# Optimization experiments

Measured on AMD Instinct MI355X. Metric: run time of the kernel, lower is better.

Reference implementation:

```python
import jax, jax.numpy as jnp
import numpy as np

E = 128      # embedding_dim
H = 128      # hidden_dim
A = 4        # n_ary
DEPTH = 8    # complete 4-ary tree depth (root at level 0)
N_NODES = (A ** (DEPTH + 1) - 1) // (A - 1)  # 87381


def setup_inputs() -> dict:
    key = jax.random.key(0)
    ks = jax.random.split(key, 11)
    s = 0.05  # weight scale to keep gates in a sane range
    return {
        "embeddings": jax.random.normal(ks[0], (N_NODES, E), jnp.float32),
        "W_iou": jax.random.normal(ks[1], (3 * H, E), jnp.float32) * s,
        "b_iou": jax.random.normal(ks[2], (3 * H,), jnp.float32) * s,
        "U_iou": jax.random.normal(ks[3], (3 * H, A * H), jnp.float32) * s,
        "b_uiou": jax.random.normal(ks[4], (3 * H,), jnp.float32) * s,
        "W_f": jax.random.normal(ks[5], (H, E), jnp.float32) * s,
        "b_wf": jax.random.normal(ks[6], (H,), jnp.float32) * s,
        "U_f": jax.random.normal(ks[7], (A * H, A * H), jnp.float32) * s,
        "b_uf": jax.random.normal(ks[8], (A * H,), jnp.float32) * s,
        "h0": jax.random.uniform(ks[9], (1, A * H), jnp.float32),
        "c0": jax.random.uniform(ks[10], (1, A * H), jnp.float32),
    }


def _tree_lstm_cell(x, h, c, W_iou, b_iou, U_iou, b_uiou, W_f, b_wf, U_f, b_uf):
    # x: [n, E], h/c: [n, A*H]
    n = x.shape[0]
    iou = x @ W_iou.T + b_iou + h @ U_iou.T + b_uiou          # [n, 3H]
    i, o, u = jnp.split(iou, 3, axis=1)
    # forget gates: one per child slot, broadcast W_f(x) over arity dim
    f = jax.nn.sigmoid((h @ U_f.T + b_uf).reshape(n, A, H)
                       + (x @ W_f.T + b_wf)[:, None, :])       # [n, A, H]
    c_new = jax.nn.sigmoid(i) * jnp.tanh(u) + jnp.sum(f * c.reshape(n, A, H), axis=1)
    h_new = jax.nn.sigmoid(o) * jnp.tanh(c_new)
    return h_new, c_new


def reference(embeddings, W_iou, b_iou, U_iou, b_uiou, W_f, b_wf, U_f, b_uf, h0, c0):
    # Level-synchronized bottom-up pass over a complete 4-ary tree of depth DEPTH.
    # embeddings are ordered deepest-level-first; children of parent i at level l
    # are nodes 4i..4i+3 of level l+1.
    hs, cs = [], []
    off = 0
    n_leaf = A ** DEPTH
    h_in = jnp.tile(h0, (n_leaf, 1))  # leaves use learned initial state
    c_in = jnp.tile(c0, (n_leaf, 1))
    for l in range(DEPTH, -1, -1):
        n = A ** l
        x = embeddings[off:off + n]
        h_new, c_new = _tree_lstm_cell(x, h_in, c_in,
                                       W_iou, b_iou, U_iou, b_uiou,
                                       W_f, b_wf, U_f, b_uf)
        hs.append(h_new)
        cs.append(c_new)
        off += n
        if l > 0:
            # pack each parent's A children states into one [A*H] vector
            h_in = h_new.reshape(n // A, A * H)
            c_in = c_new.reshape(n // A, A * H)
    out_h = jnp.concatenate(hs, axis=0)[None]  # [1, N_NODES, H]
    out_c = jnp.concatenate(cs, axis=0)[None]  # [1, N_NODES, H]
    return out_h, out_c
```

## Files before the change

### kernel.cpp

```cpp
#include <hip/hip_runtime.h>
#include <hip/hip_bf16.h>

#define DEPTH   8
#define NNODES  87381
#define KIN     640
#define NOUTS   896
#define CT_STRIDE 10240
#define KT_STRIDE 512

typedef __attribute__((ext_vector_type(8))) unsigned short ushort8;
typedef __attribute__((ext_vector_type(4))) unsigned short ushort4v;
typedef __attribute__((ext_vector_type(8))) __bf16        bf16x8;
typedef __attribute__((ext_vector_type(4))) float         f32x4;

union Frag8 { ushort8 u; bf16x8 b; };

__device__ __forceinline__ unsigned short f2bf(float f) {
    unsigned int x = __float_as_uint(f);
    x += 0x7fffu + ((x >> 16) & 1u);
    return (unsigned short)(x >> 16);
}
__device__ __forceinline__ float sigf(float x) {
    return __builtin_amdgcn_rcpf(1.0f + __expf(-x));
}
__device__ __forceinline__ float tanh_fast(float x) { return 2.0f * sigf(2.0f * x) - 1.0f; }

__global__ __launch_bounds__(256) void build_wc(
    const float* __restrict__ W_iou, const float* __restrict__ U_iou,
    const float* __restrict__ W_f,   const float* __restrict__ U_f,
    unsigned short* __restrict__ Wc)
{
    int idx = blockIdx.x * 256 + threadIdx.x;
    int ct  = idx / CT_STRIDE;
    int r1  = idx - ct * CT_STRIDE;
    int kt  = r1 >> 9;
    int r2  = r1 & 511;
    int ln  = r2 >> 3;
    int j   = r2 & 7;
    int out = ct * 16 + (ln & 15);
    int k   = kt * 32 + ((ln >> 4) << 3) + j;
    float v;
    if (out < 384) {
        v = (k < 128) ? W_iou[out * 128 + k] : U_iou[(size_t)out * 512 + (k - 128)];
    } else {
        int o2 = out - 384;
        v = (k < 128) ? W_f[(o2 & 127) * 128 + k] : U_f[(size_t)o2 * 512 + (k - 128)];
    }
    Wc[idx] = f2bf(v);
}

__global__ __launch_bounds__(64) void build_consts(
    const float* __restrict__ U_iou, const float* __restrict__ U_f,
    const float* __restrict__ b_iou, const float* __restrict__ b_uiou,
    const float* __restrict__ b_wf,  const float* __restrict__ b_uf,
    const float* __restrict__ h0,
    float* __restrict__ biasc, float* __restrict__ hUc)
{
    int o = blockIdx.x * 64 + threadIdx.x;
    if (o >= NOUTS) return;
    float b = (o < 384) ? (b_iou[o] + b_uiou[o])
                        : (b_wf[(o - 384) & 127] + b_uf[o - 384]);
    const float* Urow = (o < 384) ? (U_iou + (size_t)o * 512)
                                  : (U_f + (size_t)(o - 384) * 512);
    float s0 = 0.f, s1 = 0.f, s2 = 0.f, s3 = 0.f;
    #pragma unroll 2
    for (int k = 0; k < 512; k += 16) {
        float4 u0 = *(const float4*)(Urow + k);
        float4 h0v = *(const float4*)(h0 + k);
        float4 u1 = *(const float4*)(Urow + k + 4);
        float4 h1v = *(const float4*)(h0 + k + 4);
        float4 u2 = *(const float4*)(Urow + k + 8);
        float4 h2v = *(const float4*)(h0 + k + 8);
        float4 u3 = *(const float4*)(Urow + k + 12);
        float4 h3v = *(const float4*)(h0 + k + 12);
        s0 += u0.x*h0v.x + u0.y*h0v.y + u0.z*h0v.z + u0.w*h0v.w;
        s1 += u1.x*h1v.x + u1.y*h1v.y + u1.z*h1v.z + u1.w*h1v.w;
        s2 += u2.x*h2v.x + u2.y*h2v.y + u2.z*h2v.z + u2.w*h2v.w;
        s3 += u3.x*h3v.x + u3.y*h3v.y + u3.z*h3v.z + u3.w*h3v.w;
    }
    biasc[o] = b;
    hUc[o]   = b + ((s0 + s1) + (s2 + s3));
}

__device__ __forceinline__ void tile_body(
    const float* __restrict__ emb,
    const unsigned short* __restrict__ Wc,
    const float* __restrict__ biasc, const float* __restrict__ hUc,
    const float* __restrict__ c0,
    float* __restrict__ outh, float* __restrict__ outc,
    char* lds,
    int n, int off, int cb, int leaf, int node0)
{
    const int tid  = threadIdx.x;
    const int srow = tid >> 3;
    const int skq  = (tid & 7) << 3;
    const unsigned swz = (unsigned)((srow * 128 + skq * 2) ^ ((srow & 7) << 4));
    int r = node0 + srow; if (r >= n) r = n - 1;

    const int wv  = tid >> 6;
    const int ln  = tid & 63;
    const int grp = ln >> 4;
    const int cl  = ln & 15;

    const int nsteps = leaf ? 2 : 10;

    f32x4 acc[4][7] = {};
    float4 pv0, pv1;

    auto issue = [&](int ks) {
        const int k = ks * 64 + skq;
        const float* src;
        if (leaf || k < 128) {
            src = emb + (size_t)(off + r) * 128 + k;
        } else {
            const int khm = k - 128;
            const int a = khm >> 7, d0 = khm & 127;
            src = outh + (size_t)(cb + 4 * r + a) * 128 + d0;
        }
        pv0 = *(const float4*)(src);
        pv1 = *(const float4*)(src + 4);
    };
    auto pack_write = [&](char* buf) {
        ushort8 w;
        w[0] = f2bf(pv0.x); w[1] = f2bf(pv0.y); w[2] = f2bf(pv0.z); w[3] = f2bf(pv0.w);
        w[4] = f2bf(pv1.x); w[5] = f2bf(pv1.y); w[6] = f2bf(pv1.z); w[7] = f2bf(pv1.w);
        *(ushort8*)(buf + swz) = w;
    };

    const unsigned short* wp[7];
    #pragma unroll
    for (int cf = 0; cf < 7; ++cf) {
        const int ct = cf * 8 + wv;
        wp[cf] = Wc + (size_t)ct * CT_STRIDE + (size_t)ln * 8;
    }

    issue(0);
    pack_write(lds);
    for (int ks = 0; ks < nsteps; ++ks) {
        char* cur = lds + (size_t)(ks & 1) * 8192;
        if (ks + 1 < nsteps) issue(ks + 1);
        __syncthreads();
        #pragma unroll
        for (int kc = 0; kc < 2; ++kc) {
            const int kt = ks * 2 + kc;
            Frag8 bfr[7];
            #pragma unroll
            for (int cf = 0; cf < 7; ++cf)
                bfr[cf].u = *(const ushort8*)(wp[cf] + kt * KT_STRIDE);
            #pragma unroll
            for (int rf = 0; rf < 4; ++rf) {
                const int row = rf * 16 + cl;
                const unsigned rby = (unsigned)(row * 128 + kc * 64 + grp * 16) ^ ((row & 7) << 4);
                Frag8 afr; afr.u = *(const ushort8*)(cur + rby);
                #pragma unroll
                for (int cf = 0; cf < 7; ++cf)
                    acc[rf][cf] = __builtin_amdgcn_mfma_f32_16x16x32_bf16(
                        afr.b, bfr[cf].b, acc[rf][cf], 0, 0, 0);
            }
        }
        if (ks + 1 < nsteps) pack_write(lds + (size_t)((ks + 1) & 1) * 8192);
    }
    __syncthreads();

    const float* bv = leaf ? hUc : biasc;
    const int d = wv * 16 + cl;
    const float bi = bv[d];
    const float bo = bv[128 + d];
    const float bu = bv[256 + d];
    float bfa[4], cin_leaf[4];
    #pragma unroll
    for (int a = 0; a < 4; ++a) bfa[a] = bv[384 + a * 128 + d];
    if (leaf) {
        #pragma unroll
        for (int a = 0; a < 4; ++a) cin_leaf[a] = c0[a * 128 + d];
    }

    #pragma unroll
    for (int rf = 0; rf < 4; ++rf) {
        #pragma unroll
        for (int reg = 0; reg < 4; ++reg) {
            const int m = node0 + rf * 16 + grp * 4 + reg;
            if (m < n) {
                const float i_ = acc[rf][0][reg] + bi;
                const float o_ = acc[rf][1][reg] + bo;
                const float u_ = acc[rf][2][reg] + bu;
                float c_ = sigf(i_) * tanh_fast(u_);
                #pragma unroll
                for (int a = 0; a < 4; ++a) {
                    const float fp = acc[rf][3 + a][reg] + bfa[a];
                    const float cin = leaf ? cin_leaf[a]
                                           : outc[(size_t)(cb + 4 * m + a) * 128 + d];
                    c_ += sigf(fp) * cin;
                }
                const float h_ = sigf(o_) * tanh_fast(c_);
                const size_t oidx = (size_t)(off + m) * 128 + d;
                outh[oidx] = h_;
                outc[oidx] = c_;
            }
        }
    }
}

__global__ __launch_bounds__(512) void tree_level(
    const float* __restrict__ emb, const unsigned short* __restrict__ Wc,
    const float* __restrict__ biasc, const float* __restrict__ hUc,
    const float* __restrict__ c0,
    float* __restrict__ outh, float* __restrict__ outc,
    int n, int off, int cb, int leaf)
{
    __shared__ __align__(16) char lds[2 * 8192];
    tile_body(emb, Wc, biasc, hUc, c0, outh, outc, lds, n, off, cb, leaf,
              blockIdx.x * 64);
}

__global__ __launch_bounds__(512) void tree_dsplit(
    const float* __restrict__ emb, const unsigned short* __restrict__ Wc,
    const float* __restrict__ biasc,
    float* __restrict__ outh, float* __restrict__ outc,
    int n, int off, int cb)
{
    __shared__ __align__(16) char lds[57344];

    const int tid   = threadIdx.x;
    const int mt    = blockIdx.x >> 3;
    const int dg    = blockIdx.x & 7;
    const int node0 = mt * 32;

    {
        const int srow = tid >> 4;
        const int sc4  = (tid & 15) << 2;
        int r = node0 + srow; if (r >= n) r = n - 1;
        const unsigned wby = (unsigned)((srow * 128 + sc4 * 2) ^ ((srow & 7) << 4));
        float4 v[10];
        #pragma unroll
        for (int i = 0; i < 10; ++i) {
            const int k = i * 64 + sc4;
            const float* src = (k < 128)
                ? (emb + (size_t)(off + r) * 128 + k)
                : (outh + (size_t)(cb + 4 * r + ((k - 128) >> 7)) * 128 + ((k - 128) & 127));
            v[i] = *(const float4*)src;
        }
        #pragma unroll
        for (int i = 0; i < 10; ++i) {
            ushort4v w;
            w[0] = f2bf(v[i].x); w[1] = f2bf(v[i].y);
            w[2] = f2bf(v[i].z); w[3] = f2bf(v[i].w);
            *(ushort4v*)(lds + i * 4096 + wby) = w;
        }
    }
    __syncthreads();

    const int wv  = tid >> 6;
    const int ln  = tid & 63;
    const int grp = ln >> 4;
    const int cl  = ln & 15;
    const int rf  = wv & 1;
    const int kq  = wv >> 1;
    const int row = rf * 16 + cl;
    const int swr = (row & 7) << 4;

    const unsigned short* wp[7];
    #pragma unroll
    for (int cf = 0; cf < 7; ++cf)
        wp[cf] = Wc + (size_t)(cf * 8 + dg) * CT_STRIDE + (size_t)ln * 8;

    f32x4 acc[7] = {};
    #pragma unroll
    for (int t = 0; t < 5; ++t) {
        const int kt = kq * 5 + t;
        Frag8 afr;
        afr.u = *(const ushort8*)(lds + (kt >> 1) * 4096 + row * 128
                                  + (((kt & 1) * 64 + grp * 16) ^ swr));
        Frag8 bfr[7];
        #pragma unroll
        for (int cf = 0; cf < 7; ++cf)
            bfr[cf].u = *(const ushort8*)(wp[cf] + (size_t)kt * KT_STRIDE);
        #pragma unroll
        for (int cf = 0; cf < 7; ++cf)
            acc[cf] = __builtin_amdgcn_mfma_f32_16x16x32_bf16(
                afr.b, bfr[cf].b, acc[cf], 0, 0, 0);
    }
    __syncthreads();

    float* red = (float*)lds;
    const int slot = ((kq * 2 + rf) * 64 + ln) * 28;
    if (kq != 0) {
        #pragma unroll
        for (int cf = 0; cf < 7; ++cf)
            *(f32x4*)(red + slot + cf * 4) = acc[cf];
    }
    __syncthreads();
    if (kq == 0) {
        #pragma unroll
        for (int q = 1; q < 4; ++q) {
            const int s2 = ((q * 2 + rf) * 64 + ln) * 28;
            #pragma unroll
            for (int cf = 0; cf < 7; ++cf)
                acc[cf] += *(const f32x4*)(red + s2 + cf * 4);
        }

        const int d = dg * 16 + cl;
        const float bi = biasc[d];
        const float bo = biasc[128 + d];
        const float bu = biasc[256 + d];
        float bfa[4];
        #pragma unroll
        for (int a = 0; a < 4; ++a) bfa[a] = biasc[384 + a * 128 + d];

        #pragma unroll
        for (int reg = 0; reg < 4; ++reg) {
            const int m = node0 + rf * 16 + grp * 4 + reg;
            if (m < n) {
                const float i_ = acc[0][reg] + bi;
                const float o_ = acc[1][reg] + bo;
                const float u_ = acc[2][reg] + bu;
                float c_ = sigf(i_) * tanh_fast(u_);
                #pragma unroll
                for (int a = 0; a < 4; ++a) {
                    const float fp = acc[3 + a][reg] + bfa[a];
                    const float cin = outc[(size_t)(cb + 4 * m + a) * 128 + d];
                    c_ += sigf(fp) * cin;
                }
                const float h_ = sigf(o_) * tanh_fast(c_);
                const size_t oidx = (size_t)(off + m) * 128 + d;
                outh[oidx] = h_;
                outc[oidx] = c_;
            }
        }
    }
}

extern "C" void kernel_launch(void* const* d_in, const int* in_sizes, int n_in,
                              void* d_out, int out_size, void* d_ws, size_t ws_size,
                              hipStream_t stream)
{
    const float* emb    = (const float*)d_in[0];
    const float* W_iou  = (const float*)d_in[1];
    const float* b_iou  = (const float*)d_in[2];
    const float* U_iou  = (const float*)d_in[3];
    const float* b_uiou = (const float*)d_in[4];
    const float* W_f    = (const float*)d_in[5];
    const float* b_wf   = (const float*)d_in[6];
    const float* U_f    = (const float*)d_in[7];
    const float* b_uf   = (const float*)d_in[8];
    const float* h0     = (const float*)d_in[9];
    const float* c0     = (const float*)d_in[10];

    unsigned short* Wc = (unsigned short*)d_ws;
    float* biasc = (float*)((char*)d_ws + (size_t)NOUTS * KIN * 2);
    float* hUc   = biasc + NOUTS;

    hipLaunchKernelGGL(build_wc, dim3((NOUTS * KIN) / 256), dim3(256), 0, stream,
                       W_iou, U_iou, W_f, U_f, Wc);
    hipLaunchKernelGGL(build_consts, dim3((NOUTS + 63) / 64), dim3(64), 0, stream,
                       U_iou, U_f, b_iou, b_uiou, b_wf, b_uf, h0, biasc, hUc);

    float* outh = (float*)d_out;
    float* outc = outh + (size_t)NNODES * 128;

    int off = 0, cb = 0;
    for (int l = DEPTH; l >= 0; --l) {
        const int n = 1 << (2 * l);
        if (l >= DEPTH - 1) {
            const int nb = (n + 63) / 64;
            hipLaunchKernelGGL(tree_level, dim3(nb), dim3(512), 0, stream,
                               emb, Wc, biasc, hUc, c0, outh, outc,
                               n, off, cb, (l == DEPTH) ? 1 : 0);
        } else {
            const int nb = ((n + 31) / 32) * 8;
            hipLaunchKernelGGL(tree_dsplit, dim3(nb), dim3(512), 0, stream,
                               emb, Wc, biasc, outh, outc, n, off, cb);
        }
        cb = off;
        off += n;
    }
}
```

Baseline: 279.6 us.

## Fuse upper tree levels into cooperative kernel and cache child h as bf16

Levels 6 through 0 now run in one cooperative persistent kernel with grid.sync between levels, replacing seven separate launches. The leaf and level-7 passes get dedicated kernels. Every level also writes a bf16 copy of h, so parents can load child states directly as bf16 instead of reading and converting fp32. The cost is an extra bf16 write per node and grid-wide barriers. A fallback to per-level launches runs if the cooperative launch fails.

```diff
diff --git a/kernel.cpp b/kernel.cpp
--- a/kernel.cpp
+++ b/kernel.cpp
@@ -1,5 +1,8 @@
 #include <hip/hip_runtime.h>
 #include <hip/hip_bf16.h>
+#include <hip/hip_cooperative_groups.h>
+
+namespace cg = cooperative_groups;
 
 #define DEPTH   8
 #define NNODES  87381
@@ -62,62 +65,41 @@
                         : (b_wf[(o - 384) & 127] + b_uf[o - 384]);
     const float* Urow = (o < 384) ? (U_iou + (size_t)o * 512)
                                   : (U_f + (size_t)(o - 384) * 512);
-    float s0 = 0.f, s1 = 0.f, s2 = 0.f, s3 = 0.f;
-    #pragma unroll 2
-    for (int k = 0; k < 512; k += 16) {
+    float s0 = 0.f, s1 = 0.f;
+    #pragma unroll 4
+    for (int k = 0; k < 512; k += 8) {
         float4 u0 = *(const float4*)(Urow + k);
-        float4 h0v = *(const float4*)(h0 + k);
+        float4 hv0 = *(const float4*)(h0 + k);
         float4 u1 = *(const float4*)(Urow + k + 4);
-        float4 h1v = *(const float4*)(h0 + k + 4);
-        float4 u2 = *(const float4*)(Urow + k + 8);
-        float4 h2v = *(const float4*)(h0 + k + 8);
-        float4 u3 = *(const float4*)(Urow + k + 12);
-        float4 h3v = *(const float4*)(h0 + k + 12);
-        s0 += u0.x*h0v.x + u0.y*h0v.y + u0.z*h0v.z + u0.w*h0v.w;
-        s1 += u1.x*h1v.x + u1.y*h1v.y + u1.z*h1v.z + u1.w*h1v.w;
-        s2 += u2.x*h2v.x + u2.y*h2v.y + u2.z*h2v.z + u2.w*h2v.w;
-        s3 += u3.x*h3v.x + u3.y*h3v.y + u3.z*h3v.z + u3.w*h3v.w;
+        float4 hv1 = *(const float4*)(h0 + k + 4);
+        s0 += u0.x*hv0.x + u0.y*hv0.y + u0.z*hv0.z + u0.w*hv0.w;
+        s1 += u1.x*hv1.x + u1.y*hv1.y + u1.z*hv1.z + u1.w*hv1.w;
     }
     biasc[o] = b;
-    hUc[o]   = b + ((s0 + s1) + (s2 + s3));
-}
-
-__device__ __forceinline__ void tile_body(
-    const float* __restrict__ emb,
-    const unsigned short* __restrict__ Wc,
-    const float* __restrict__ biasc, const float* __restrict__ hUc,
-    const float* __restrict__ c0,
+    hUc[o]   = b + s0 + s1;
+}
+
+__global__ __launch_bounds__(512) void tree_leaf(
+    const float* __restrict__ emb, const unsigned short* __restrict__ Wc,
+    const float* __restrict__ hUc, const float* __restrict__ c0,
     float* __restrict__ outh, float* __restrict__ outc,
-    char* lds,
-    int n, int off, int cb, int leaf, int node0)
-{
-    const int tid  = threadIdx.x;
-    const int srow = tid >> 3;
-    const int skq  = (tid & 7) << 3;
+    unsigned short* __restrict__ hb, int n)
+{
+    __shared__ __align__(16) char lds[2 * 8192];
+    const int tid   = threadIdx.x;
+    const int node0 = blockIdx.x * 64;
+    const int srow  = tid >> 3;
+    const int skq   = (tid & 7) << 3;
     const unsigned swz = (unsigned)((srow * 128 + skq * 2) ^ ((srow & 7) << 4));
     int r = node0 + srow; if (r >= n) r = n - 1;
 
-    const int wv  = tid >> 6;
-    const int ln  = tid & 63;
-    const int grp = ln >> 4;
-    const int cl  = ln & 15;
-
-    const int nsteps = leaf ? 2 : 10;
+    const int wv = tid >> 6, ln = tid & 63, grp = ln >> 4, cl = ln & 15;
 
     f32x4 acc[4][7] = {};
     float4 pv0, pv1;
-
     auto issue = [&](int ks) {
-        const int k = ks * 64 + skq;
-        const float* src;
-        if (leaf || k < 128) {
-            src = emb + (size_t)(off + r) * 128 + k;
-        } else {
-            const int khm = k - 128;
-            const int a = khm >> 7, d0 = khm & 127;
-            src = outh + (size_t)(cb + 4 * r + a) * 128 + d0;
-        }
-        pv0 = *(const float4*)(src);
+        const float* src = emb + (size_t)r * 128 + ks * 64 + skq;
+        pv0 = *(const float4*)src;
         pv1 = *(const float4*)(src + 4);
     };
     auto pack_write = [&](char* buf) {
@@ -129,16 +111,15 @@
 
     const unsigned short* wp[7];
     #pragma unroll
-    for (int cf = 0; cf < 7; ++cf) {
-        const int ct = cf * 8 + wv;
-        wp[cf] = Wc + (size_t)ct * CT_STRIDE + (size_t)ln * 8;
-    }
+    for (int cf = 0; cf < 7; ++cf)
+        wp[cf] = Wc + (size_t)(cf * 8 + wv) * CT_STRIDE + (size_t)ln * 8;
 
     issue(0);
     pack_write(lds);
-    for (int ks = 0; ks < nsteps; ++ks) {
+    #pragma unroll
+    for (int ks = 0; ks < 2; ++ks) {
         char* cur = lds + (size_t)(ks & 1) * 8192;
-        if (ks + 1 < nsteps) issue(ks + 1);
+        if (ks == 0) issue(1);
         __syncthreads();
         #pragma unroll
         for (int kc = 0; kc < 2; ++kc) {
@@ -158,22 +139,16 @@
                         afr.b, bfr[cf].b, acc[rf][cf], 0, 0, 0);
             }
         }
-        if (ks + 1 < nsteps) pack_write(lds + (size_t)((ks + 1) & 1) * 8192);
-    }
-    __syncthreads();
-
-    const float* bv = leaf ? hUc : biasc;
+        if (ks == 0) pack_write(lds + 8192);
+    }
+
     const int d = wv * 16 + cl;
-    const float bi = bv[d];
-    const float bo = bv[128 + d];
-    const float bu = bv[256 + d];
+    const float bi = hUc[d];
+    const float bo = hUc[128 + d];
+    const float bu = hUc[256 + d];
     float bfa[4], cin_leaf[4];
     #pragma unroll
-    for (int a = 0; a < 4; ++a) bfa[a] = bv[384 + a * 128 + d];
-    if (leaf) {
-        #pragma unroll
-        for (int a = 0; a < 4; ++a) cin_leaf[a] = c0[a * 128 + d];
-    }
+    for (int a = 0; a < 4; ++a) { bfa[a] = hUc[384 + a * 128 + d]; cin_leaf[a] = c0[a * 128 + d]; }
 
     #pragma unroll
     for (int rf = 0; rf < 4; ++rf) {
@@ -186,44 +161,26 @@
                 const float u_ = acc[rf][2][reg] + bu;
                 float c_ = sigf(i_) * tanh_fast(u_);
                 #pragma unroll
-                for (int a = 0; a < 4; ++a) {
-                    const float fp = acc[rf][3 + a][reg] + bfa[a];
-                    const float cin = leaf ? cin_leaf[a]
-                                           : outc[(size_t)(cb + 4 * m + a) * 128 + d];
-                    c_ += sigf(fp) * cin;
-                }
+                for (int a = 0; a < 4; ++a)
+                    c_ += sigf(acc[rf][3 + a][reg] + bfa[a]) * cin_leaf[a];
                 const float h_ = sigf(o_) * tanh_fast(c_);
-                const size_t oidx = (size_t)(off + m) * 128 + d;
+                const size_t oidx = (size_t)m * 128 + d;
                 outh[oidx] = h_;
                 outc[oidx] = c_;
+                hb[oidx]   = f2bf(h_);
             }
         }
     }
 }
 
-__global__ __launch_bounds__(512) void tree_level(
-    const float* __restrict__ emb, const unsigned short* __restrict__ Wc,
-    const float* __restrict__ biasc, const float* __restrict__ hUc,
-    const float* __restrict__ c0,
-    float* __restrict__ outh, float* __restrict__ outc,
-    int n, int off, int cb, int leaf)
-{
-    __shared__ __align__(16) char lds[2 * 8192];
-    tile_body(emb, Wc, biasc, hUc, c0, outh, outc, lds, n, off, cb, leaf,
-              blockIdx.x * 64);
-}
-
-__global__ __launch_bounds__(512) void tree_dsplit(
+__device__ __forceinline__ void dsplit_unit(
     const float* __restrict__ emb, const unsigned short* __restrict__ Wc,
     const float* __restrict__ biasc,
     float* __restrict__ outh, float* __restrict__ outc,
-    int n, int off, int cb)
-{
-    __shared__ __align__(16) char lds[57344];
-
+    unsigned short* __restrict__ hb,
+    char* lds, int n, int off, int cb, int mt, int dg)
+{
     const int tid   = threadIdx.x;
-    const int mt    = blockIdx.x >> 3;
-    const int dg    = blockIdx.x & 7;
     const int node0 = mt * 32;
 
     {
@@ -231,22 +188,18 @@
         const int sc4  = (tid & 15) << 2;
         int r = node0 + srow; if (r >= n) r = n - 1;
         const unsigned wby = (unsigned)((srow * 128 + sc4 * 2) ^ ((srow & 7) << 4));
-        float4 v[10];
-        #pragma unroll
-        for (int i = 0; i < 10; ++i) {
-            const int k = i * 64 + sc4;
-            const float* src = (k < 128)
-                ? (emb + (size_t)(off + r) * 128 + k)
-                : (outh + (size_t)(cb + 4 * r + ((k - 128) >> 7)) * 128 + ((k - 128) & 127));
-            v[i] = *(const float4*)src;
-        }
-        #pragma unroll
-        for (int i = 0; i < 10; ++i) {
-            ushort4v w;
-            w[0] = f2bf(v[i].x); w[1] = f2bf(v[i].y);
-            w[2] = f2bf(v[i].z); w[3] = f2bf(v[i].w);
-            *(ushort4v*)(lds + i * 4096 + wby) = w;
-        }
+        ushort4v w[10];
+        const float4 v0 = *(const float4*)(emb + (size_t)(off + r) * 128 + sc4);
+        const float4 v1 = *(const float4*)(emb + (size_t)(off + r) * 128 + 64 + sc4);
+        #pragma unroll
+        for (int i = 2; i < 10; ++i)
+            w[i] = *(const ushort4v*)(hb + (size_t)(cb + 4 * r + ((i - 2) >> 1)) * 128
+                                         + ((i - 2) & 1) * 64 + sc4);
+        w[0][0] = f2bf(v0.x); w[0][1] = f2bf(v0.y); w[0][2] = f2bf(v0.z); w[0][3] = f2bf(v0.w);
+        w[1][0] = f2bf(v1.x); w[1][1] = f2bf(v1.y); w[1][2] = f2bf(v1.z); w[1][3] = f2bf(v1.w);
+        #pragma unroll
+        for (int i = 0; i < 10; ++i)
+            *(ushort4v*)(lds + i * 4096 + wby) = w[i];
     }
     __syncthreads();
 
@@ -298,7 +251,6 @@
             for (int cf = 0; cf < 7; ++cf)
                 acc[cf] += *(const f32x4*)(red + s2 + cf * 4);
         }
-
         const int d = dg * 16 + cl;
         const float bi = biasc[d];
         const float bo = biasc[128 + d];
@@ -316,17 +268,52 @@
                 const float u_ = acc[2][reg] + bu;
                 float c_ = sigf(i_) * tanh_fast(u_);
                 #pragma unroll
-                for (int a = 0; a < 4; ++a) {
-                    const float fp = acc[3 + a][reg] + bfa[a];
-                    const float cin = outc[(size_t)(cb + 4 * m + a) * 128 + d];
-                    c_ += sigf(fp) * cin;
-                }
+                for (int a = 0; a < 4; ++a)
+                    c_ += sigf(acc[3 + a][reg] + bfa[a]) * outc[(size_t)(cb + 4 * m + a) * 128 + d];
                 const float h_ = sigf(o_) * tanh_fast(c_);
                 const size_t oidx = (size_t)(off + m) * 128 + d;
                 outh[oidx] = h_;
                 outc[oidx] = c_;
+                hb[oidx]   = f2bf(h_);
             }
         }
+    }
+}
+
+__global__ __launch_bounds__(512) void tree_dsplit(
+    const float* __restrict__ emb, const unsigned short* __restrict__ Wc,
+    const float* __restrict__ biasc,
+    float* __restrict__ outh, float* __restrict__ outc,
+    unsigned short* __restrict__ hb,
+    int n, int off, int cb)
+{
+    __shared__ __align__(16) char lds[57344];
+    dsplit_unit(emb, Wc, biasc, outh, outc, hb, lds, n, off, cb,
+                blockIdx.x >> 3, blockIdx.x & 7);
+}
+
+__global__ __launch_bounds__(512) void tree_coop(
+    const float* __restrict__ emb, const unsigned short* __restrict__ Wc,
+    const float* __restrict__ biasc,
+    float* __restrict__ outh, float* __restrict__ outc,
+    unsigned short* __restrict__ hb)
+{
+    __shared__ __align__(16) char lds[57344];
+    const int ns[7]   = {4096, 1024, 256, 64, 16, 4, 1};
+    const int offs[7] = {81920, 86016, 87040, 87296, 87360, 87376, 87380};
+    const int cbs[7]  = {65536, 81920, 86016, 87040, 87296, 87360, 87376};
+    cg::grid_group grid = cg::this_grid();
+    #pragma unroll 1
+    for (int li = 0; li < 7; ++li) {
+        const int n = ns[li], off = offs[li], cb = cbs[li];
+        const int units = ((n + 31) >> 5) * 8;
+        for (int u = blockIdx.x; u < units; u += gridDim.x) {
+            dsplit_unit(emb, Wc, biasc, outh, outc, hb, lds, n, off, cb,
+                        u >> 3, u & 7);
+            __syncthreads();
+        }
+        __threadfence();
+        grid.sync();
     }
 }
 
@@ -349,6 +336,8 @@
     unsigned short* Wc = (unsigned short*)d_ws;
     float* biasc = (float*)((char*)d_ws + (size_t)NOUTS * KIN * 2);
     float* hUc   = biasc + NOUTS;
+    unsigned short* hb = (unsigned short*)((char*)d_ws + (size_t)NOUTS * KIN * 2
+                                           + 2 * NOUTS * sizeof(float));
 
     hipLaunchKernelGGL(build_wc, dim3((NOUTS * KIN) / 256), dim3(256), 0, stream,
                        W_iou, U_iou, W_f, U_f, Wc);
@@ -358,20 +347,28 @@
     float* outh = (float*)d_out;
     float* outc = outh + (size_t)NNODES * 128;
 
-    int off = 0, cb = 0;
-    for (int l = DEPTH; l >= 0; --l) {
-        const int n = 1 << (2 * l);
-        if (l >= DEPTH - 1) {
-            const int nb = (n + 63) / 64;
-            hipLaunchKernelGGL(tree_level, dim3(nb), dim3(512), 0, stream,
-                               emb, Wc, biasc, hUc, c0, outh, outc,
-                               n, off, cb, (l == DEPTH) ? 1 : 0);
-        } else {
-            const int nb = ((n + 31) / 32) * 8;
+    hipLaunchKernelGGL(tree_leaf, dim3(1024), dim3(512), 0, stream,
+                       emb, Wc, hUc, c0, outh, outc, hb, 65536);
+    hipLaunchKernelGGL(tree_dsplit, dim3(4096), dim3(512), 0, stream,
+                       emb, Wc, biasc, outh, outc, hb, 16384, 65536, 0);
+
+    const float* a_emb = emb; const unsigned short* a_wc = Wc;
+    const float* a_biasc = biasc; float* a_outh = outh; float* a_outc = outc;
+    unsigned short* a_hb = hb;
+    void* cargs[] = {(void*)&a_emb, (void*)&a_wc, (void*)&a_biasc,
+                     (void*)&a_outh, (void*)&a_outc, (void*)&a_hb};
+    hipError_t ce = hipLaunchCooperativeKernel((const void*)tree_coop,
+                                               dim3(256), dim3(512), cargs, 0, stream);
+    if (ce != hipSuccess) {
+        (void)hipGetLastError();
+        const int ns[7]   = {4096, 1024, 256, 64, 16, 4, 1};
+        const int offs[7] = {81920, 86016, 87040, 87296, 87360, 87376, 87380};
+        const int cbs[7]  = {65536, 81920, 86016, 87040, 87296, 87360, 87376};
+        for (int li = 0; li < 7; ++li) {
+            const int nb = ((ns[li] + 31) / 32) * 8;
             hipLaunchKernelGGL(tree_dsplit, dim3(nb), dim3(512), 0, stream,
-                               emb, Wc, biasc, outh, outc, n, off, cb);
-        }
-        cb = off;
-        off += n;
-    }
-}
+                               emb, Wc, biasc, outh, outc, hb,
+                               ns[li], offs[li], cbs[li]);
+        }
+    }
+}
```

After: 775.4 us. +177.4%, slower.
